# Optimization experiments

Hardware: AMD Instinct MI355X
Metric: run time of the kernel (lower is better)

The kernel has to match this reference:

```python
import jax, jax.numpy as jnp
import numpy as np

EMBED = 1024
HEADS = 16
DEPTH = EMBED // HEADS
FFN_DIM = 4096
EPS = 1e-9


def layer_norm(x, g, b):
    mu = jnp.mean(x, axis=-1, keepdims=True)
    var = jnp.mean(jnp.square(x - mu), axis=-1, keepdims=True)
    return (x - mu) * jax.lax.rsqrt(var + EPS) * g + b


def setup_inputs() -> dict:
    key = jax.random.key(0)
    ks = jax.random.split(key, 16)
    B, S = 2, 2048
    s_e = 1.0 / np.sqrt(EMBED)
    s_f = 1.0 / np.sqrt(FFN_DIM)
    return {
        "x": jax.random.normal(ks[0], (B, S, EMBED), dtype=jnp.float32),
        "mask": jnp.zeros((B, 1, 1, S), dtype=jnp.float32),
        "wq_w": jax.random.normal(ks[1], (EMBED, EMBED), dtype=jnp.float32) * s_e,
        "wq_b": jnp.zeros((EMBED,), dtype=jnp.float32),
        "wk_w": jax.random.normal(ks[2], (EMBED, EMBED), dtype=jnp.float32) * s_e,
        "wk_b": jnp.zeros((EMBED,), dtype=jnp.float32),
        "wv_w": jax.random.normal(ks[3], (EMBED, EMBED), dtype=jnp.float32) * s_e,
        "wv_b": jnp.zeros((EMBED,), dtype=jnp.float32),
        "wo_w": jax.random.normal(ks[4], (EMBED, EMBED), dtype=jnp.float32) * s_e,
        "wo_b": jnp.zeros((EMBED,), dtype=jnp.float32),
        "f1_w": jax.random.normal(ks[5], (EMBED, FFN_DIM), dtype=jnp.float32) * s_e,
        "f1_b": jnp.zeros((FFN_DIM,), dtype=jnp.float32),
        "f2_w": jax.random.normal(ks[6], (FFN_DIM, EMBED), dtype=jnp.float32) * s_f,
        "f2_b": jnp.zeros((EMBED,), dtype=jnp.float32),
        "ln1_g": jnp.ones((EMBED,), dtype=jnp.float32),
        "ln1_b": jnp.zeros((EMBED,), dtype=jnp.float32),
        "ln2_g": jnp.ones((EMBED,), dtype=jnp.float32),
        "ln2_b": jnp.zeros((EMBED,), dtype=jnp.float32),
    }


def reference(x, mask, wq_w, wq_b, wk_w, wk_b, wv_w, wv_b, wo_w, wo_b,
              f1_w, f1_b, f2_w, f2_b, ln1_g, ln1_b, ln2_g, ln2_b):
    B, S, E = x.shape

    def split_heads(t):  # (B,S,E) -> (B,H,S,D)
        return t.reshape(B, S, HEADS, DEPTH).transpose(0, 2, 1, 3)

    q = split_heads(x @ wq_w + wq_b)
    k = split_heads(x @ wk_w + wk_b)
    v = split_heads(x @ wv_w + wv_b)

    logits = jnp.einsum("bhqd,bhkd->bhqk", q, k) / jnp.sqrt(jnp.float32(DEPTH))
    logits = logits + mask * -1e12  # mask broadcast (B,1,1,S)
    attn = jax.nn.softmax(logits, axis=-1)
    out = jnp.einsum("bhqk,bhkd->bhqd", attn, v)
    out = out.transpose(0, 2, 1, 3).reshape(B, S, E)
    out = out @ wo_w + wo_b

    # dropout is identity (is_train=False)
    h = layer_norm(out + x, ln1_g, ln1_b)
    f = jax.nn.relu(h @ f1_w + f1_b) @ f2_w + f2_b
    return layer_norm(f + h, ln2_g, ln2_b)
```

## Files before the change

kernel.cpp:

```cpp
#include <hip/hip_runtime.h>
#include <hip/hip_bf16.h>
#include <stdint.h>

typedef __hip_bfloat16 bf16;
typedef __attribute__((ext_vector_type(8))) short short8;
typedef __attribute__((ext_vector_type(4))) short short4v;
typedef __attribute__((ext_vector_type(4))) float floatx4;

#define E_DIM 1024
#define S_LEN 2048
#define NB    2
#define NH    16
#define HD    64
#define FFN   4096
#define MTOT  4096

__device__ __forceinline__ void gl_lds16(const void* g, void* l) {
  __builtin_amdgcn_global_load_lds(
      (__attribute__((address_space(1))) void*)(g),
      (__attribute__((address_space(3))) void*)(l), 16, 0, 0);
}

__device__ __forceinline__ int fswz_v(int row) { return row & 7; }
__device__ __forceinline__ int fswz_k(int row) {
  return ((row ^ (row >> 3)) & 3) | ((((row >> 3) ^ (row >> 4)) & 1) << 2);
}

__device__ __forceinline__ float bf16bits2float(short s) {
  union { unsigned u; float f; } c;
  c.u = ((unsigned)(unsigned short)s) << 16;
  return c.f;
}

__global__ __launch_bounds__(256)
void cvt_bf16(const float* __restrict__ in, bf16* __restrict__ out) {
  const size_t i = ((size_t)blockIdx.x * 256 + threadIdx.x) * 4;
  float4 v = *(const float4*)(in + i);
  out[i + 0] = __float2bfloat16(v.x);
  out[i + 1] = __float2bfloat16(v.y);
  out[i + 2] = __float2bfloat16(v.z);
  out[i + 3] = __float2bfloat16(v.w);
}

__global__ __launch_bounds__(256)
void transpose_all(const float* __restrict__ wq, const float* __restrict__ wk,
                   const float* __restrict__ wv, const float* __restrict__ wo,
                   const float* __restrict__ f1, const float* __restrict__ f2,
                   bf16* __restrict__ W3T, bf16* __restrict__ woT,
                   bf16* __restrict__ f1T, bf16* __restrict__ f2T) {
  const int z = blockIdx.z;
  const float* in;
  bf16* out;
  int inStride, outStride, rOff, cOff;
  if (z < 4) {
    in = (z == 0) ? wq : (z == 1) ? wk : (z == 2) ? wv : wo;
    out = (z < 3) ? (W3T + (size_t)z * 1024 * 1024) : woT;
    inStride = 1024; outStride = 1024; rOff = 0; cOff = 0;
  } else if (z < 8) {
    in = f1; out = f1T; inStride = 4096; outStride = 1024;
    rOff = 0; cOff = (z - 4) * 1024;
  } else {
    in = f2; out = f2T; inStride = 1024; outStride = 4096;
    rOff = (z - 8) * 1024; cOff = 0;
  }
  __shared__ float tile[32][33];
  const int tx = threadIdx.x & 31;
  const int ty = threadIdx.x >> 5;
  const int c0 = blockIdx.x * 32;
  const int r0 = blockIdx.y * 32;
#pragma unroll
  for (int j = 0; j < 32; j += 8)
    tile[ty + j][tx] =
        in[(size_t)(rOff + r0 + ty + j) * inStride + cOff + c0 + tx];
  __syncthreads();
#pragma unroll
  for (int j = 0; j < 32; j += 8)
    out[(size_t)(cOff + c0 + ty + j) * outStride + rOff + r0 + tx] =
        __float2bfloat16(tile[tx][ty + j]);
}

__global__ __launch_bounds__(256)
void prep_bias(const float* __restrict__ qb, const float* __restrict__ kb,
               const float* __restrict__ vb, float* __restrict__ out) {
  const int i = blockIdx.x * 256 + threadIdx.x;
  float v = (i < 1024) ? qb[i] * 0.125f
                       : ((i < 2048) ? kb[i - 1024] : vb[i - 2048]);
  out[i] = v;
}

__global__ __launch_bounds__(512)
void gemm256(const bf16* __restrict__ A, const bf16* __restrict__ B,
             const float* __restrict__ bias, void* __restrict__ Cout,
             void* __restrict__ Cout2,
             int M, int N, int Kpart, int lda, int mode) {
  __shared__ alignas(16) bf16 sA[2][256 * 32];
  __shared__ alignas(16) bf16 sB[2][256 * 32];
  const int tid   = threadIdx.x;
  const int wave  = tid >> 6;
  const int lane  = tid & 63;
  const int row16 = lane & 15;
  const int quad  = lane >> 4;

  const int gx = gridDim.x;
  const int nwg = gx * gridDim.y;
  const int cpx = nwg >> 3;
  int id = blockIdx.y * gx + blockIdx.x;
  id = (id & 7) * cpx + (id >> 3);
  const int m0 = (id % gx) * 256;
  const int n0 = (id / gx) * 256;

  const int wm = (wave >> 2) * 128;
  const int wn = (wave & 3) * 64;
  const int koff = blockIdx.z * Kpart;
  const int NT = Kpart >> 5;

  floatx4 acc[8][4];
#pragma unroll
  for (int i = 0; i < 8; i++)
#pragma unroll
    for (int j = 0; j < 4; j++) {
      floatx4 z = {0.f, 0.f, 0.f, 0.f};
      acc[i][j] = z;
    }

  auto stage = [&](int t, int p) {
    const int k0 = koff + t * 32;
#pragma unroll
    for (int j = 0; j < 2; ++j) {
      const int seg = wave * 2 + j;
      const int r = seg * 16 + (lane >> 2);
      const int c = (lane & 3) * 8;
      gl_lds16(A + (size_t)(m0 + r) * lda + k0 + c, &sA[p][seg * 512]);
      gl_lds16(B + (size_t)(n0 + r) * lda + k0 + c, &sB[p][seg * 512]);
    }
  };

  auto compute = [&](int p) {
    const bf16* sAp = sA[p];
    const bf16* sBp = sB[p];
    short8 bfr[4];
#pragma unroll
    for (int ni = 0; ni < 4; ni++)
      bfr[ni] = *(const short8*)(sBp + (wn + ni * 16 + row16) * 32 + quad * 8);
    __builtin_amdgcn_s_setprio(1);
#pragma unroll
    for (int mi = 0; mi < 8; mi++) {
      short8 af = *(const short8*)(sAp + (wm + mi * 16 + row16) * 32 + quad * 8);
#pragma unroll
      for (int ni = 0; ni < 4; ni++)
        acc[mi][ni] = __builtin_amdgcn_mfma_f32_16x16x32_bf16(
            af, bfr[ni], acc[mi][ni], 0, 0, 0);
    }
    __builtin_amdgcn_s_setprio(0);
  };

  stage(0, 0);
  stage(1, 1);
  asm volatile("s_waitcnt vmcnt(4)" ::: "memory");
  __builtin_amdgcn_sched_barrier(0);
  asm volatile("s_barrier" ::: "memory");

  for (int t = 0; t < NT; ++t) {
    const int p = t & 1;
    compute(p);
    asm volatile("s_waitcnt lgkmcnt(0)" ::: "memory");
    __builtin_amdgcn_sched_barrier(0);
    asm volatile("s_barrier" ::: "memory");
    if (t + 2 < NT) {
      stage(t + 2, p);
      asm volatile("s_waitcnt vmcnt(4)" ::: "memory");
    } else {
      asm volatile("s_waitcnt vmcnt(0)" ::: "memory");
    }
    __builtin_amdgcn_sched_barrier(0);
    asm volatile("s_barrier" ::: "memory");
  }

  float bval[4] = {0.f, 0.f, 0.f, 0.f};
  if (mode != 0) {
#pragma unroll
    for (int ni = 0; ni < 4; ni++) bval[ni] = bias[n0 + wn + ni * 16 + row16];
  }

#pragma unroll
  for (int mi = 0; mi < 8; mi++) {
#pragma unroll
    for (int ni = 0; ni < 4; ni++) {
      const int col = n0 + wn + ni * 16 + row16;
      if (mode == 0) {
        float* co = (float*)((blockIdx.z < 2) ? Cout : Cout2) +
                    (size_t)(blockIdx.z & 1) * M * N;
#pragma unroll
        for (int r = 0; r < 4; r++) {
          const int row = m0 + wm + mi * 16 + quad * 4 + r;
          co[(size_t)row * N + col] = acc[mi][ni][r];
        }
      } else if (mode == 1) {
#pragma unroll
        for (int r = 0; r < 4; r++) {
          const int row = m0 + wm + mi * 16 + quad * 4 + r;
          float v = acc[mi][ni][r] + bval[ni];
          v = v > 0.f ? v : 0.f;
          ((bf16*)Cout)[(size_t)row * N + col] = __float2bfloat16(v);
        }
      } else {
        const int mat = col >> 10;
        const int c10 = col & 1023;
        const int hh = c10 >> 6, dd = c10 & 63;
        const float scl = (mat == 0) ? 0.125f : 1.0f;
        bf16* qout = (bf16*)Cout;
        const int rbase = m0 + wm + mi * 16 + quad * 4;
        const int b = rbase >> 11, s = rbase & 2047;
        const size_t bh = (size_t)b * NH + hh;
        if (mat == 2) {
          bf16* vt = qout + (1 << 23);
          short4v pv;
#pragma unroll
          for (int r = 0; r < 4; r++) {
            bf16 t = __float2bfloat16(acc[mi][ni][r] + bval[ni]);
            pv[r] = *(short*)&t;
          }
          *(short4v*)(vt + (bh * HD + dd) * S_LEN + s) = pv;
        } else {
          bf16* o = (mat == 1) ? (qout + (1 << 22)) : qout;
#pragma unroll
          for (int r = 0; r < 4; r++) {
            float v = acc[mi][ni][r] * scl + bval[ni];
            o[(bh * S_LEN + s + r) * HD + dd] = __float2bfloat16(v);
          }
        }
      }
    }
  }
}

__global__ __launch_bounds__(256, 4)
void flash_attn(const bf16* __restrict__ Q, const bf16* __restrict__ K,
                const bf16* __restrict__ Vt, const float* __restrict__ mask,
                bf16* __restrict__ Out) {
  __shared__ alignas(16) bf16 sK[64 * 64];
  __shared__ alignas(16) bf16 sV[64 * 64];
  __shared__ alignas(16) float sM[S_LEN];

  const int tid   = threadIdx.x;
  const int wave  = tid >> 6;
  const int lane  = tid & 63;
  const int row16 = lane & 15;
  const int quad  = lane >> 4;
  const int bh = blockIdx.y;
  const int b = bh >> 4, h = bh & 15;
  const int q0 = blockIdx.x * 64;
  const int qg = q0 + wave * 16 + row16;

  const bf16* qp = Q + ((size_t)bh * S_LEN + qg) * HD;
  short8 qf0 = *(const short8*)(qp + quad * 8);
  short8 qf1 = *(const short8*)(qp + 32 + quad * 8);

  for (int i = tid; i < S_LEN / 4; i += 256) {
    float4 mv = ((const float4*)(mask + (size_t)b * S_LEN))[i];
    float4 w = {-1e12f * mv.x, -1e12f * mv.y, -1e12f * mv.z, -1e12f * mv.w};
    ((float4*)sM)[i] = w;
  }

  float m_i = -1e30f, l_i = 0.f;
  floatx4 ov[4];
#pragma unroll
  for (int i = 0; i < 4; i++) { floatx4 z = {0.f,0.f,0.f,0.f}; ov[i] = z; }

  const bf16* Kbase = K + (size_t)bh * S_LEN * HD;
  const bf16* Vbase = Vt + (size_t)bh * HD * S_LEN;

  for (int kt = 0; kt < S_LEN / 64; ++kt) {
    const bf16* Kg = Kbase + (size_t)kt * 64 * HD;
    const bf16* Vg = Vbase + kt * 64;
#pragma unroll
    for (int j = 0; j < 2; ++j) {
      const int ch = wave * 2 + j;
      const int row = ch * 8 + (lane >> 3);
      const int sc_ = lane & 7;
      gl_lds16(Kg + row * 64 + ((sc_ ^ fswz_k(row)) * 8), sK + ch * 512);
      gl_lds16(Vg + (size_t)row * S_LEN + ((sc_ ^ fswz_v(row)) * 8), sV + ch * 512);
    }
    __syncthreads();

    floatx4 sc[4];
#pragma unroll
    for (int mi = 0; mi < 4; mi++) {
      const int row = ((row16 >> 2) << 3) + (row16 & 3) + ((mi & 1) << 2) + ((mi >> 1) << 5);
      const int fk = fswz_k(row);
      short8 kf0 = *(const short8*)(sK + row * 64 + ((quad ^ fk) << 3));
      short8 kf1 = *(const short8*)(sK + row * 64 + (((4 + quad) ^ fk) << 3));
      floatx4 z = {0.f, 0.f, 0.f, 0.f};
      z = __builtin_amdgcn_mfma_f32_16x16x32_bf16(kf0, qf0, z, 0, 0, 0);
      sc[mi] = __builtin_amdgcn_mfma_f32_16x16x32_bf16(kf1, qf1, z, 0, 0, 0);
    }

#pragma unroll
    for (int mi = 0; mi < 4; mi++) {
      float4 mv = *(const float4*)(sM + kt * 64 + (quad << 3) + ((mi & 1) << 2) + ((mi >> 1) << 5));
      sc[mi][0] += mv.x; sc[mi][1] += mv.y; sc[mi][2] += mv.z; sc[mi][3] += mv.w;
    }

    float t = sc[0][0];
#pragma unroll
    for (int mi = 0; mi < 4; mi++)
#pragma unroll
      for (int r = 0; r < 4; r++) t = fmaxf(t, sc[mi][r]);
    t = fmaxf(t, __shfl_xor(t, 16));
    t = fmaxf(t, __shfl_xor(t, 32));
    const float m_new = fmaxf(m_i, t);
    const float alpha = __expf(m_i - m_new);
    m_i = m_new;
    float tsum = 0.f;
#pragma unroll
    for (int mi = 0; mi < 4; mi++)
#pragma unroll
      for (int r = 0; r < 4; r++) {
        float p = __expf(sc[mi][r] - m_new);
        sc[mi][r] = p;
        tsum += p;
      }
    tsum += __shfl_xor(tsum, 16);
    tsum += __shfl_xor(tsum, 32);
    l_i = l_i * alpha + tsum;

    short8 pf[2];
#pragma unroll
    for (int ks = 0; ks < 2; ks++)
#pragma unroll
      for (int jp = 0; jp < 4; jp++) {
        const int mi = 2 * ks + (jp >> 1);
        const int r0 = (jp & 1) * 2;
        bf16 p0 = __float2bfloat16(sc[mi][r0]);
        bf16 p1 = __float2bfloat16(sc[mi][r0 + 1]);
        pf[ks][2 * jp]     = *(short*)&p0;
        pf[ks][2 * jp + 1] = *(short*)&p1;
      }

#pragma unroll
    for (int mi = 0; mi < 4; mi++)
#pragma unroll
      for (int r = 0; r < 4; r++) ov[mi][r] *= alpha;
#pragma unroll
    for (int mi = 0; mi < 4; mi++) {
      const int row = mi * 16 + row16;
      const int fv = fswz_v(row);
      short8 v0 = *(const short8*)(sV + row * 64 + ((quad ^ fv) << 3));
      short8 v1 = *(const short8*)(sV + row * 64 + (((4 + quad) ^ fv) << 3));
      ov[mi] = __builtin_amdgcn_mfma_f32_16x16x32_bf16(v0, pf[0], ov[mi], 0, 0, 0);
      ov[mi] = __builtin_amdgcn_mfma_f32_16x16x32_bf16(v1, pf[1], ov[mi], 0, 0, 0);
    }
    __syncthreads();
  }

  const float inv = 1.0f / l_i;
#pragma unroll
  for (int mi = 0; mi < 4; mi++) {
    short4v pv;
#pragma unroll
    for (int r = 0; r < 4; r++) {
      bf16 t = __float2bfloat16(ov[mi][r] * inv);
      pv[r] = *(short*)&t;
    }
    *(short4v*)(Out + ((size_t)(b * S_LEN + qg)) * E_DIM + h * HD + mi * 16 + quad * 4) = pv;
  }
}

__global__ __launch_bounds__(256)
void ln_reduce(const float* __restrict__ p0, const float* __restrict__ p1,
               const float* __restrict__ p2, const float* __restrict__ p3,
               const float* __restrict__ resf, const bf16* __restrict__ resb,
               const float* __restrict__ bias, const float* __restrict__ g,
               const float* __restrict__ be, float* __restrict__ outf,
               bf16* __restrict__ outb) {
  const int row = blockIdx.x;
  const int tid = threadIdx.x;
  const size_t base = (size_t)row * 1024;
  const int c = tid * 4;
  float4 a = *(const float4*)(p0 + base + c);
  float4 bq = *(const float4*)(p1 + base + c);
  float4 xv;
  xv.x = a.x + bq.x;
  xv.y = a.y + bq.y;
  xv.z = a.z + bq.z;
  xv.w = a.w + bq.w;
  if (p2) {
    float4 a2 = *(const float4*)(p2 + base + c);
    float4 a3 = *(const float4*)(p3 + base + c);
    xv.x += a2.x + a3.x;
    xv.y += a2.y + a3.y;
    xv.z += a2.z + a3.z;
    xv.w += a2.w + a3.w;
  }
  float4 rv;
  if (resf) {
    rv = *(const float4*)(resf + base + c);
  } else {
    short4v rb = *(const short4v*)((const short*)resb + base + c);
    rv.x = bf16bits2float(rb[0]);
    rv.y = bf16bits2float(rb[1]);
    rv.z = bf16bits2float(rb[2]);
    rv.w = bf16bits2float(rb[3]);
  }
  float4 bi = *(const float4*)(bias + c);
  xv.x += rv.x + bi.x;
  xv.y += rv.y + bi.y;
  xv.z += rv.z + bi.z;
  xv.w += rv.w + bi.w;
  float s  = xv.x + xv.y + xv.z + xv.w;
  float s2 = xv.x * xv.x + xv.y * xv.y + xv.z * xv.z + xv.w * xv.w;
#pragma unroll
  for (int d = 1; d < 64; d <<= 1) {
    s  += __shfl_xor(s, d);
    s2 += __shfl_xor(s2, d);
  }
  __shared__ float red[2][4];
  const int wave = tid >> 6;
  if ((tid & 63) == 0) { red[0][wave] = s; red[1][wave] = s2; }
  __syncthreads();
  s  = red[0][0] + red[0][1] + red[0][2] + red[0][3];
  s2 = red[1][0] + red[1][1] + red[1][2] + red[1][3];
  const float mu  = s * (1.0f / 1024.0f);
  const float var = s2 * (1.0f / 1024.0f) - mu * mu;
  const float rs  = rsqrtf(var + 1e-9f);
  float4 gg = *(const float4*)(g + c);
  float4 bb = *(const float4*)(be + c);
  float4 y;
  y.x = (xv.x - mu) * rs * gg.x + bb.x;
  y.y = (xv.y - mu) * rs * gg.y + bb.y;
  y.z = (xv.z - mu) * rs * gg.z + bb.z;
  y.w = (xv.w - mu) * rs * gg.w + bb.w;
  if (outf) *(float4*)(outf + base + c) = y;
  if (outb) {
    bf16* o = outb + base + c;
    o[0] = __float2bfloat16(y.x);
    o[1] = __float2bfloat16(y.y);
    o[2] = __float2bfloat16(y.z);
    o[3] = __float2bfloat16(y.w);
  }
}

extern "C" void kernel_launch(void* const* d_in, const int* in_sizes, int n_in,
                              void* d_out, int out_size, void* d_ws,
                              size_t ws_size, hipStream_t stream) {
  const float* x    = (const float*)d_in[0];
  const float* mask = (const float*)d_in[1];
  const float* wq_w = (const float*)d_in[2];
  const float* wq_b = (const float*)d_in[3];
  const float* wk_w = (const float*)d_in[4];
  const float* wk_b = (const float*)d_in[5];
  const float* wv_w = (const float*)d_in[6];
  const float* wv_b = (const float*)d_in[7];
  const float* wo_w = (const float*)d_in[8];
  const float* wo_b = (const float*)d_in[9];
  const float* f1_w = (const float*)d_in[10];
  const float* f1_b = (const float*)d_in[11];
  const float* f2_w = (const float*)d_in[12];
  const float* f2_b = (const float*)d_in[13];
  const float* ln1_g = (const float*)d_in[14];
  const float* ln1_b = (const float*)d_in[15];
  const float* ln2_g = (const float*)d_in[16];
  const float* ln2_b = (const float*)d_in[17];
  float* out = (float*)d_out;

  char* ws = (char*)d_ws;
  const size_t MB = 1u << 20;
  bf16*  xbf   = (bf16*)(ws + 0 * MB);
  bf16*  W3T   = (bf16*)(ws + 8 * MB);
  bf16*  woT   = (bf16*)(ws + 14 * MB);
  float* bqkv  = (float*)(ws + 16 * MB);
  bf16*  Qb    = (bf16*)(ws + 17 * MB);
  bf16*  attnb = (bf16*)(ws + 0 * MB);
  bf16*  ffn1  = (bf16*)(ws + 17 * MB);
  bf16*  f1T   = (bf16*)(ws + 49 * MB);
  bf16*  f2T   = (bf16*)(ws + 57 * MB);
  float* P01   = (float*)(ws + 65 * MB);
  bf16*  hbf   = (bf16*)(ws + 97 * MB);
  float* P23   = (float*)(ws + 105 * MB);
  const size_t PS = (size_t)MTOT * E_DIM;

  const int KS = (ws_size >= (size_t)137 * MB) ? 4 : 2;
  const float* p2 = (KS == 4) ? P23 : nullptr;
  const float* p3 = (KS == 4) ? P23 + PS : nullptr;

  cvt_bf16<<<4096, 256, 0, stream>>>(x, xbf);
  transpose_all<<<dim3(32, 32, 12), 256, 0, stream>>>(
      wq_w, wk_w, wv_w, wo_w, f1_w, f2_w, W3T, woT, f1T, f2T);
  prep_bias<<<12, 256, 0, stream>>>(wq_b, wk_b, wv_b, bqkv);

  gemm256<<<dim3(16, 12, 1), 512, 0, stream>>>(
      xbf, W3T, bqkv, Qb, nullptr, MTOT, 3 * E_DIM, E_DIM, E_DIM, 2);

  flash_attn<<<dim3(S_LEN / 64, NB * NH), 256, 0, stream>>>(
      Qb, Qb + (1 << 22), Qb + (1 << 23), mask, attnb);

  gemm256<<<dim3(16, 4, KS), 512, 0, stream>>>(
      attnb, woT, nullptr, P01, P23, MTOT, E_DIM, E_DIM / KS, E_DIM, 0);

  ln_reduce<<<MTOT, 256, 0, stream>>>(P01, P01 + PS, p2, p3, x, nullptr,
                                      wo_b, ln1_g, ln1_b, nullptr, hbf);

  gemm256<<<dim3(16, 16, 1), 512, 0, stream>>>(
      hbf, f1T, f1_b, ffn1, nullptr, MTOT, FFN, E_DIM, E_DIM, 1);

  gemm256<<<dim3(16, 4, KS), 512, 0, stream>>>(
      ffn1, f2T, nullptr, P01, P23, MTOT, E_DIM, FFN / KS, FFN, 0);

  ln_reduce<<<MTOT, 256, 0, stream>>>(P01, P01 + PS, p2, p3, nullptr, hbf,
                                      f2_b, ln2_g, ln2_b, out, nullptr);
}
```

Before: 409.3 us.

## Restructure GEMM mainloop with 64-wide K tiles, XOR swizzle and staggered half-tile loads

The 256x256 GEMM now stages 64-wide K slices split into 128-row halves with an XOR-swizzled LDS layout, and interleaves global-to-LDS loads of the next slices between four MFMA quadrant phases. This is meant to reduce LDS bank conflicts, halve the number of barrier-delimited iterations, and overlap memory traffic with compute more finely. LDS use doubles to 128KB per block, and launch bounds now request 2 waves per EU. The extra barriers and the larger register footprint for holding fragments could limit occupancy or add stalls.

```diff
diff --git a/kernel.cpp b/kernel.cpp
--- a/kernel.cpp
+++ b/kernel.cpp
@@ -20,6 +20,12 @@
       (__attribute__((address_space(1))) void*)(g),
       (__attribute__((address_space(3))) void*)(l), 16, 0, 0);
 }
+
+#define VMW(N)  do { asm volatile("s_waitcnt vmcnt(" #N ")" ::: "memory"); \
+                     __builtin_amdgcn_sched_barrier(0); } while (0)
+#define LGKM0   do { asm volatile("s_waitcnt lgkmcnt(0)" ::: "memory"); \
+                     __builtin_amdgcn_sched_barrier(0); } while (0)
+#define BARR    do { asm volatile("s_barrier" ::: "memory"); } while (0)
 
 __device__ __forceinline__ int fswz_v(int row) { return row & 7; }
 __device__ __forceinline__ int fswz_k(int row) {
@@ -88,18 +94,19 @@
   out[i] = v;
 }
 
-__global__ __launch_bounds__(512)
+__global__ __launch_bounds__(512, 2)
 void gemm256(const bf16* __restrict__ A, const bf16* __restrict__ B,
              const float* __restrict__ bias, void* __restrict__ Cout,
              void* __restrict__ Cout2,
              int M, int N, int Kpart, int lda, int mode) {
-  __shared__ alignas(16) bf16 sA[2][256 * 32];
-  __shared__ alignas(16) bf16 sB[2][256 * 32];
+  __shared__ alignas(16) bf16 sA[2][2][128 * 64];
+  __shared__ alignas(16) bf16 sB[2][2][128 * 64];
   const int tid   = threadIdx.x;
   const int wave  = tid >> 6;
   const int lane  = tid & 63;
   const int row16 = lane & 15;
   const int quad  = lane >> 4;
+  const int sw7   = row16 & 7;
 
   const int gx = gridDim.x;
   const int nwg = gx * gridDim.y;
@@ -109,10 +116,14 @@
   const int m0 = (id % gx) * 256;
   const int n0 = (id / gx) * 256;
 
-  const int wm = (wave >> 2) * 128;
-  const int wn = (wave & 3) * 64;
+  const int wm2 = wave >> 2;
+  const int wn4 = wave & 3;
+  const int wm  = wm2 * 128;
+  const int wn  = wn4 * 64;
+  const int hB  = wn4 >> 1;
+  const int rbB = (wn4 & 1) * 64;
   const int koff = blockIdx.z * Kpart;
-  const int NT = Kpart >> 5;
+  const int NS = Kpart >> 6;
 
   floatx4 acc[8][4];
 #pragma unroll
@@ -123,57 +134,87 @@
       acc[i][j] = z;
     }
 
-  auto stage = [&](int t, int p) {
-    const int k0 = koff + t * 32;
+  auto stage_half = [&](const bf16* G, int rowBase, int k0, bf16* dst) {
 #pragma unroll
     for (int j = 0; j < 2; ++j) {
-      const int seg = wave * 2 + j;
-      const int r = seg * 16 + (lane >> 2);
-      const int c = (lane & 3) * 8;
-      gl_lds16(A + (size_t)(m0 + r) * lda + k0 + c, &sA[p][seg * 512]);
-      gl_lds16(B + (size_t)(n0 + r) * lda + k0 + c, &sB[p][seg * 512]);
+      const int r = wave * 16 + j * 8 + (lane >> 3);
+      const int g = (lane & 7) ^ (r & 7);
+      gl_lds16(G + (size_t)(rowBase + r) * lda + k0 + g * 8,
+               dst + (wave * 16 + j * 8) * 64);
     }
   };
 
-  auto compute = [&](int p) {
-    const bf16* sAp = sA[p];
-    const bf16* sBp = sB[p];
-    short8 bfr[4];
-#pragma unroll
-    for (int ni = 0; ni < 4; ni++)
-      bfr[ni] = *(const short8*)(sBp + (wn + ni * 16 + row16) * 32 + quad * 8);
+  short8 aF[8][2];
+  short8 bF[4][2];
+  const bf16* aH = nullptr;
+  const bf16* bH = nullptr;
+
+  auto read_aF = [&](int mi0) {
+#pragma unroll
+    for (int mi = 0; mi < 4; ++mi)
+#pragma unroll
+      for (int kk = 0; kk < 2; ++kk)
+        aF[mi0 + mi][kk] = *(const short8*)(
+            aH + ((mi0 + mi) * 16 + row16) * 64 + (((kk * 4 + quad) ^ sw7) << 3));
+  };
+  auto read_bF = [&](int ni0) {
+#pragma unroll
+    for (int ni = 0; ni < 2; ++ni)
+#pragma unroll
+      for (int kk = 0; kk < 2; ++kk)
+        bF[ni0 + ni][kk] = *(const short8*)(
+            bH + (rbB + (ni0 + ni) * 16 + row16) * 64 + (((kk * 4 + quad) ^ sw7) << 3));
+  };
+  auto qmf = [&](int mi0, int ni0) {
     __builtin_amdgcn_s_setprio(1);
 #pragma unroll
-    for (int mi = 0; mi < 8; mi++) {
-      short8 af = *(const short8*)(sAp + (wm + mi * 16 + row16) * 32 + quad * 8);
-#pragma unroll
-      for (int ni = 0; ni < 4; ni++)
-        acc[mi][ni] = __builtin_amdgcn_mfma_f32_16x16x32_bf16(
-            af, bfr[ni], acc[mi][ni], 0, 0, 0);
-    }
+    for (int mi = 0; mi < 4; ++mi)
+#pragma unroll
+      for (int ni = 0; ni < 2; ++ni)
+#pragma unroll
+        for (int kk = 0; kk < 2; ++kk)
+          acc[mi0 + mi][ni0 + ni] = __builtin_amdgcn_mfma_f32_16x16x32_bf16(
+              aF[mi0 + mi][kk], bF[ni0 + ni][kk], acc[mi0 + mi][ni0 + ni], 0, 0, 0);
     __builtin_amdgcn_s_setprio(0);
   };
 
-  stage(0, 0);
-  stage(1, 1);
-  asm volatile("s_waitcnt vmcnt(4)" ::: "memory");
-  __builtin_amdgcn_sched_barrier(0);
-  asm volatile("s_barrier" ::: "memory");
-
-  for (int t = 0; t < NT; ++t) {
-    const int p = t & 1;
-    compute(p);
-    asm volatile("s_waitcnt lgkmcnt(0)" ::: "memory");
-    __builtin_amdgcn_sched_barrier(0);
-    asm volatile("s_barrier" ::: "memory");
-    if (t + 2 < NT) {
-      stage(t + 2, p);
-      asm volatile("s_waitcnt vmcnt(4)" ::: "memory");
+  stage_half(A, m0,       koff,      &sA[0][0][0]);
+  stage_half(A, m0 + 128, koff,      &sA[0][1][0]);
+  stage_half(B, n0,       koff,      &sB[0][0][0]);
+  stage_half(B, n0 + 128, koff,      &sB[0][1][0]);
+  stage_half(A, m0,       koff + 64, &sA[1][0][0]);
+  stage_half(A, m0 + 128, koff + 64, &sA[1][1][0]);
+
+  for (int s = 0; s < NS; ++s) {
+    const int b = s & 1;
+    aH = &sA[b][wm2][0];
+    bH = &sB[b][hB][0];
+    const int kn1 = koff + (s + 1) * 64;
+    const int kn2 = koff + (s + 2) * 64;
+    if (s + 1 < NS) {
+      stage_half(B, n0, kn1, &sB[(s + 1) & 1][0][0]);
+      VMW(6);
     } else {
-      asm volatile("s_waitcnt vmcnt(0)" ::: "memory");
-    }
-    __builtin_amdgcn_sched_barrier(0);
-    asm volatile("s_barrier" ::: "memory");
+      VMW(0);
+    }
+    BARR;
+    read_aF(0);
+    read_bF(0);
+    LGKM0;
+    qmf(0, 0);
+    BARR;
+    if (s + 1 < NS) stage_half(B, n0 + 128, kn1, &sB[(s + 1) & 1][1][0]);
+    read_aF(4);
+    LGKM0;
+    qmf(4, 0);
+    BARR;
+    if (s + 2 < NS) stage_half(A, m0, kn2, &sA[b][0][0]);
+    read_bF(2);
+    LGKM0;
+    qmf(0, 2);
+    BARR;
+    if (s + 2 < NS) stage_half(A, m0 + 128, kn2, &sA[b][1][0]);
+    qmf(4, 2);
   }
 
   float bval[4] = {0.f, 0.f, 0.f, 0.f};
@@ -210,8 +251,8 @@
         const float scl = (mat == 0) ? 0.125f : 1.0f;
         bf16* qout = (bf16*)Cout;
         const int rbase = m0 + wm + mi * 16 + quad * 4;
-        const int b = rbase >> 11, s = rbase & 2047;
-        const size_t bh = (size_t)b * NH + hh;
+        const int b2 = rbase >> 11, ss = rbase & 2047;
+        const size_t bh = (size_t)b2 * NH + hh;
         if (mat == 2) {
           bf16* vt = qout + (1 << 23);
           short4v pv;
@@ -220,13 +261,13 @@
             bf16 t = __float2bfloat16(acc[mi][ni][r] + bval[ni]);
             pv[r] = *(short*)&t;
           }
-          *(short4v*)(vt + (bh * HD + dd) * S_LEN + s) = pv;
+          *(short4v*)(vt + (bh * HD + dd) * S_LEN + ss) = pv;
         } else {
           bf16* o = (mat == 1) ? (qout + (1 << 22)) : qout;
 #pragma unroll
           for (int r = 0; r < 4; r++) {
             float v = acc[mi][ni][r] * scl + bval[ni];
-            o[(bh * S_LEN + s + r) * HD + dd] = __float2bfloat16(v);
+            o[(bh * S_LEN + ss + r) * HD + dd] = __float2bfloat16(v);
           }
         }
       }
```

After: 399.9 us. 1.02x faster.
